# Performance work log

Hardware: AMD Instinct MI355X
Metric: run time of the kernel (lower is better)

Reference implementation:

```python
import jax, jax.numpy as jnp
import numpy as np

N, F, H, K = 8192, 128, 128, 16
E = N * 32


def _mlp(f, w1, b1, w2, b2, w3, b3):
    h = jax.nn.relu(f @ w1 + b1)
    h = jax.nn.relu(h @ w2 + b2)
    return h @ w3 + b3


def _edge_conv(x, w1, b1, w2, b2, w3, b3, k):
    # dynamic kNN in feature space (includes self like torch_cluster.knn with x==y)
    sn = jnp.sum(x * x, axis=1)
    d = sn[:, None] + sn[None, :] - 2.0 * (x @ x.T)  # [N,N] squared dists
    idx = jax.lax.top_k(-d, k)[1]                    # [N,k] nearest neighbors
    xj = x[idx]                                      # [N,k,H]
    xi = jnp.broadcast_to(x[:, None, :], xj.shape)
    f = jnp.concatenate([xi, xj - xi], axis=-1)      # [N,k,2H]
    return jnp.max(_mlp(f, w1, b1, w2, b2, w3, b3), axis=1)  # max aggregation


def _gcn(x, w, b, src, dst, norm, n):
    h = x @ w
    out = jax.ops.segment_sum(norm[:, None] * h[src], dst, num_segments=n)
    return out + b


def _forward(x, edge_index, edge_weight,
             wg1, bg1, wg2, bg2, wg3, bg3,
             e1w1, e1b1, e1w2, e1b2, e1w3, e1b3,
             e2w1, e2b1, e2w2, e2b2, e2w3, e2b3,
             e3w1, e3b1, e3w2, e3b2, e3w3, e3b3):
    n = x.shape[0]
    loop = jnp.arange(n)
    src = jnp.concatenate([edge_index[0], loop])  # source j
    dst = jnp.concatenate([edge_index[1], loop])  # target i
    ew = jnp.concatenate([edge_weight, jnp.ones((n,), x.dtype)])  # self-loop weight 1
    deg = jax.ops.segment_sum(ew, dst, num_segments=n)
    dis = jnp.where(deg > 0, jax.lax.rsqrt(jnp.maximum(deg, 1e-12)), 0.0)
    norm = dis[src] * ew * dis[dst]

    n1 = jnp.tanh(_gcn(x, wg1, bg1, src, dst, norm, n))   # dropout is identity at eval
    e1 = _edge_conv(n1, e1w1, e1b1, e1w2, e1b2, e1w3, e1b3, K)
    e1_n1 = jnp.linalg.norm(e1 + n1, axis=1, keepdims=True)  # [N,1]

    n2 = jnp.tanh(_gcn(n1, wg2, bg2, src, dst, norm, n))
    e2 = _edge_conv(n2, e2w1, e2b1, e2w2, e2b2, e2w3, e2b3, K)
    e2_n2 = e2 + n2

    n3 = jnp.tanh(_gcn(n2, wg3, bg3, src, dst, norm, n))
    e3 = _edge_conv(n3, e3w1, e3b1, e3w2, e3b2, e3w3, e3b3, K)
    e3_n3 = e3 + n3

    x2 = e1_n1 * e2_n2 * e3_n3
    return jax.nn.log_softmax(x2, axis=1)


def setup_inputs() -> dict:
    key = jax.random.key(0)
    ks = jax.random.split(key, 32)
    inp = {
        'x': jax.random.normal(ks[0], (N, F), dtype=jnp.float32),
        'edge_index': jax.random.randint(ks[1], (2, E), 0, N, dtype=jnp.int64) if jax.config.jax_enable_x64 else jax.random.randint(ks[1], (2, E), 0, N).astype(jnp.int32),
        'edge_weight': jax.random.uniform(ks[2], (E,), dtype=jnp.float32),
    }
    s = 0.05
    gcn_in = [F, H, H]
    for i in range(3):
        inp[f'wg{i+1}'] = jax.random.normal(ks[3 + i], (gcn_in[i], H), dtype=jnp.float32) * s
        inp[f'bg{i+1}'] = jnp.zeros((H,), jnp.float32)
    dims = [(2 * H, 64), (64, H), (H, H)]
    kk = 6
    for c in range(1, 4):
        for j, (di, do) in enumerate(dims):
            inp[f'e{c}w{j+1}'] = jax.random.normal(ks[kk], (di, do), dtype=jnp.float32) * s
            inp[f'e{c}b{j+1}'] = jnp.zeros((do,), jnp.float32)
            kk += 1
    return inp


def reference(x, edge_index, edge_weight,
              wg1, bg1, wg2, bg2, wg3, bg3,
              e1w1, e1b1, e1w2, e1b2, e1w3, e1b3,
              e2w1, e2b1, e2w2, e2b2, e2w3, e2b3,
              e3w1, e3b1, e3w2, e3b2, e3w3, e3b3):
    return _forward(x, edge_index, edge_weight,
                    wg1, bg1, wg2, bg2, wg3, bg3,
                    e1w1, e1b1, e1w2, e1b2, e1w3, e1b3,
                    e2w1, e2b1, e2w2, e2b2, e2w3, e2b3,
                    e3w1, e3b1, e3w2, e3b2, e3w3, e3b3)
```

## Files before the change

### kernel.cpp

```cpp
#include <hip/hip_runtime.h>
#include <math.h>

#define N_ 8192
#define H_ 128
#define E_ 262144
#define K_ 16
#define SLABJ 1024

typedef __attribute__((ext_vector_type(8))) short bshort8;
typedef __attribute__((ext_vector_type(16))) float f32x16;
typedef unsigned long long u64;

__global__ void k_deg_init(float* deg) {
  int i = blockIdx.x * 256 + threadIdx.x;
  deg[i] = 1.0f;
}

__global__ void k_deg_scatter(const int* __restrict__ ei, const float* __restrict__ ew,
                              float* deg) {
  int e = blockIdx.x * 256 + threadIdx.x;
  atomicAdd(&deg[ei[E_ + e]], ew[e]);
}

__global__ void k_dis(float* deg) {
  int i = blockIdx.x * 256 + threadIdx.x;
  deg[i] = rsqrtf(deg[i]);
}

__global__ void k_hist(const int* __restrict__ ei, int* hist) {
  int e = blockIdx.x * 256 + threadIdx.x;
  atomicAdd(&hist[ei[E_ + e]], 1);
}

__global__ void k_scan(int* hist, int* rowptr) {
  __shared__ int part[256];
  __shared__ int partx[257];
  int t = threadIdx.x;
  int base = t * 32;
  int loc[32];
  int s = 0;
#pragma unroll
  for (int i = 0; i < 32; ++i) { loc[i] = s; s += hist[base + i]; }
  part[t] = s;
  __syncthreads();
  if (t == 0) {
    int r = 0;
    for (int i = 0; i < 256; ++i) { partx[i] = r; r += part[i]; }
    partx[256] = r;
  }
  __syncthreads();
  int b = partx[t];
#pragma unroll
  for (int i = 0; i < 32; ++i) {
    rowptr[base + i] = b + loc[i];
    hist[base + i] = b + loc[i];
  }
  if (t == 0) rowptr[N_] = partx[256];
}

__global__ void k_edgebuild(const int* __restrict__ ei, const float* __restrict__ ew,
                            const float* __restrict__ dis, int* cursor,
                            int* __restrict__ srcS, float* __restrict__ normS) {
  int e = blockIdx.x * 256 + threadIdx.x;
  int s = ei[e], d = ei[E_ + e];
  int pos = atomicAdd(&cursor[d], 1);
  srcS[pos] = s;
  normS[pos] = dis[s] * ew[e] * dis[d];
}

__device__ __forceinline__ unsigned short f2bf_rne(float x) {
  unsigned u = __builtin_bit_cast(unsigned, x);
  unsigned r = ((u >> 16) & 1u) + 0x7fffu;
  return (unsigned short)((u + r) >> 16);
}
__device__ __forceinline__ float bf2f(unsigned short b) {
  unsigned u = ((unsigned)b) << 16;
  return __builtin_bit_cast(float, u);
}

struct WP { const float* p[12]; };

__global__ void k_wprepAll(WP wp, bshort8* __restrict__ wAll) {
  int id = blockIdx.x * 256 + threadIdx.x;
  int layer = id / 7168;
  int r = id - layer * 7168;
  bshort8* base = wAll + layer * 14336;
  const float* src;
  bshort8 *dH, *dL;
  int slot, kind;
  if (r < 2048)      { kind = 0; slot = r;        src = wp.p[layer*4+0]; dH = base;         dL = base + 2048; }
  else if (r < 4096) { kind = 1; slot = r - 2048; src = wp.p[layer*4+1]; dH = base + 4096;  dL = base + 6144; }
  else if (r < 5120) { kind = 2; slot = r - 4096; src = wp.p[layer*4+2]; dH = base + 8192;  dL = base + 9216; }
  else               { kind = 3; slot = r - 5120; src = wp.p[layer*4+3]; dH = base + 10240; dL = base + 12288; }
  int lane = slot & 63;
  int n, k0;
  if (kind == 2) {
    int ks = (slot >> 6) & 3, nt = slot >> 8;
    n = nt * 32 + (lane & 31);
    k0 = ks * 16 + (lane >> 5) * 8;
  } else {
    int ks = (slot >> 6) & 7, nt = slot >> 9;
    n = nt * 32 + (lane & 31);
    k0 = ks * 16 + (lane >> 5) * 8;
  }
  bshort8 h, l;
#pragma unroll
  for (int i = 0; i < 8; ++i) {
    int k = k0 + i;
    float v;
    if (kind == 1) v = (n < 64) ? (src[k * 64 + n] - src[(128 + k) * 64 + n])
                                : src[(128 + k) * 64 + (n - 64)];
    else v = src[k * 128 + n];
    unsigned short hb = f2bf_rne(v);
    h[i] = (short)hb;
    l[i] = (short)f2bf_rne(v - bf2f(hb));
  }
  dH[slot] = h;
  dL[slot] = l;
}

__global__ __launch_bounds__(256, 3) void k_gemmM(const float* __restrict__ A,
                                                  const bshort8* __restrict__ wfH,
                                                  const bshort8* __restrict__ wfL,
                                                  float* __restrict__ C) {
  __shared__ short aHs[32 * 132], aLs[32 * 132];
  int t = threadIdx.x;
  int r0 = blockIdx.x * 32;
  int w = t >> 6, lane = t & 63, q = lane & 31, half = lane >> 5;

  {
    int r = t >> 3;
    int kc = (t & 7) * 16;
    const float* p = A + (r0 + r) * 128 + kc;
#pragma unroll
    for (int e4 = 0; e4 < 4; ++e4) {
      float4 v = *(const float4*)(p + e4 * 4);
      float vals[4] = {v.x, v.y, v.z, v.w};
      unsigned short hs[4], ls[4];
#pragma unroll
      for (int i = 0; i < 4; ++i) {
        hs[i] = f2bf_rne(vals[i]);
        ls[i] = f2bf_rne(vals[i] - bf2f(hs[i]));
      }
      int off = r * 132 + kc + e4 * 4;
      *(u64*)&aHs[off] = ((u64)hs[0]) | ((u64)hs[1] << 16) | ((u64)hs[2] << 32) | ((u64)hs[3] << 48);
      *(u64*)&aLs[off] = ((u64)ls[0]) | ((u64)ls[1] << 16) | ((u64)ls[2] << 32) | ((u64)ls[3] << 48);
    }
  }
  bshort8 bH[8], bL[8];
#pragma unroll
  for (int ks = 0; ks < 8; ++ks) {
    bH[ks] = wfH[(w * 8 + ks) * 64 + lane];
    bL[ks] = wfL[(w * 8 + ks) * 64 + lane];
  }
  __syncthreads();

  f32x16 accP, accQ;
#pragma unroll
  for (int r = 0; r < 16; ++r) { accP[r] = 0.f; accQ[r] = 0.f; }
#pragma unroll
  for (int ks = 0; ks < 8; ++ks) {
    int off = q * 132 + ks * 16 + half * 8;
    union { bshort8 v; u64 u[2]; } aH, aL;
    aH.u[0] = *(const u64*)&aHs[off];
    aH.u[1] = *(const u64*)&aHs[off + 4];
    aL.u[0] = *(const u64*)&aLs[off];
    aL.u[1] = *(const u64*)&aLs[off + 4];
    accQ = __builtin_amdgcn_mfma_f32_32x32x16_bf16(aL.v, bH[ks], accQ, 0, 0, 0);
    accQ = __builtin_amdgcn_mfma_f32_32x32x16_bf16(aH.v, bL[ks], accQ, 0, 0, 0);
    accP = __builtin_amdgcn_mfma_f32_32x32x16_bf16(aH.v, bH[ks], accP, 0, 0, 0);
  }
#pragma unroll
  for (int reg = 0; reg < 16; ++reg) {
    int row = (reg & 3) + 8 * (reg >> 2) + 4 * half;
    C[(r0 + row) * 128 + w * 32 + q] = accP[reg] + accQ[reg];
  }
}

__global__ void k_gemmMF(const bshort8* __restrict__ fAH, const bshort8* __restrict__ fAL,
                         const bshort8* __restrict__ wfH, const bshort8* __restrict__ wfL,
                         float* __restrict__ C) {
  int t = threadIdx.x;
  int rt = blockIdx.x >> 1;
  int w = (blockIdx.x & 1) * 2 + (t >> 6);
  int lane = t & 63, q = lane & 31, half = lane >> 5;

  bshort8 bH[8], bL[8], aH[8], aL[8];
#pragma unroll
  for (int ks = 0; ks < 8; ++ks) {
    bH[ks] = wfH[(w * 8 + ks) * 64 + lane];
    bL[ks] = wfL[(w * 8 + ks) * 64 + lane];
    aH[ks] = fAH[(rt * 8 + ks) * 64 + lane];
    aL[ks] = fAL[(rt * 8 + ks) * 64 + lane];
  }
  f32x16 accP, accQ;
#pragma unroll
  for (int r = 0; r < 16; ++r) { accP[r] = 0.f; accQ[r] = 0.f; }
#pragma unroll
  for (int ks = 0; ks < 8; ++ks) {
    accQ = __builtin_amdgcn_mfma_f32_32x32x16_bf16(aL[ks], bH[ks], accQ, 0, 0, 0);
    accQ = __builtin_amdgcn_mfma_f32_32x32x16_bf16(aH[ks], bL[ks], accQ, 0, 0, 0);
    accP = __builtin_amdgcn_mfma_f32_32x32x16_bf16(aH[ks], bH[ks], accP, 0, 0, 0);
  }
#pragma unroll
  for (int reg = 0; reg < 16; ++reg) {
    int row = (reg & 3) + 8 * (reg >> 2) + 4 * half;
    C[(rt * 32 + row) * 128 + w * 32 + q] = accP[reg] + accQ[reg];
  }
}

__global__ __launch_bounds__(256) void k_gcn_agg(const float* __restrict__ h,
                                                 const float* __restrict__ dis,
                                                 const int* __restrict__ rowptr,
                                                 const int* __restrict__ srcS,
                                                 const float* __restrict__ normS,
                                                 const float* __restrict__ bg,
                                                 float* __restrict__ n_out,
                                                 float* __restrict__ sn) {
  __shared__ float part[4];
  int t = threadIdx.x;
  int i = blockIdx.x * 2 + (t >> 7);
  int c = t & 127;
  float di = dis[i];
  float a0 = di * di * h[i * 128 + c], a1 = 0.f, a2 = 0.f, a3 = 0.f;
  int e0 = rowptr[i], e1 = rowptr[i + 1];
  int e = e0;
  for (; e + 4 <= e1; e += 4) {
    int s0 = srcS[e], s1 = srcS[e + 1], s2 = srcS[e + 2], s3 = srcS[e + 3];
    float w0 = normS[e], w1 = normS[e + 1], w2 = normS[e + 2], w3 = normS[e + 3];
    a0 += w0 * h[s0 * 128 + c];
    a1 += w1 * h[s1 * 128 + c];
    a2 += w2 * h[s2 * 128 + c];
    a3 += w3 * h[s3 * 128 + c];
  }
  for (; e < e1; ++e) a0 += normS[e] * h[srcS[e] * 128 + c];
  float v = tanhf(a0 + a1 + a2 + a3 + bg[c]);
  n_out[i * 128 + c] = v;
  float vv = v * v;
#pragma unroll
  for (int off = 32; off; off >>= 1) vv += __shfl_down(vv, off, 64);
  if ((t & 63) == 0) part[t >> 6] = vv;
  __syncthreads();
  if ((t & 127) == 0) sn[i] = part[t >> 6] + part[(t >> 6) + 1];
}

__global__ void k_fragprep(const float* __restrict__ src, bshort8* __restrict__ hiA,
                           bshort8* __restrict__ loA) {
  int t = blockIdx.x * 256 + threadIdx.x;
  int j = t >> 4, slot = t & 15;
  const float* p = src + j * 128 + slot * 8;
  float4 f0 = *(const float4*)p;
  float4 f1 = *(const float4*)(p + 4);
  float f[8] = {f0.x, f0.y, f0.z, f0.w, f1.x, f1.y, f1.z, f1.w};
  bshort8 h, l;
#pragma unroll
  for (int i = 0; i < 8; ++i) {
    unsigned short hb = f2bf_rne(f[i]);
    h[i] = (short)hb;
    l[i] = (short)f2bf_rne(f[i] - bf2f(hb));
  }
  int ks = slot >> 1, half = slot & 1;
  int dst = ((j >> 5) * 8 + ks) * 64 + half * 32 + (j & 31);
  hiA[dst] = h;
  loA[dst] = l;
}

__device__ __forceinline__ u64 packkey(float d, int j) {
  unsigned m = __builtin_bit_cast(unsigned, d);
  m = (m & 0x80000000u) ? ~m : (m | 0x80000000u);
  return (((u64)m) << 32) | (unsigned)j;
}

__device__ __forceinline__ float unpackd(u64 key) {
  unsigned m = (unsigned)(key >> 32);
  unsigned u = (m & 0x80000000u) ? (m & 0x7fffffffu) : ~m;
  return __builtin_bit_cast(float, u);
}

__device__ __forceinline__ void ins8(u64* tk, u64 x) {
  bool c[8];
#pragma unroll
  for (int s = 0; s < 8; ++s) c[s] = x < tk[s];
#pragma unroll
  for (int s = 7; s >= 1; --s) tk[s] = c[s - 1] ? tk[s - 1] : (c[s] ? x : tk[s]);
  tk[0] = c[0] ? x : tk[0];
}

__device__ __forceinline__ void ins16(u64* tk, u64 x) {
  bool c[16];
#pragma unroll
  for (int s = 0; s < 16; ++s) c[s] = x < tk[s];
#pragma unroll
  for (int s = 15; s >= 1; --s) tk[s] = c[s - 1] ? tk[s - 1] : (c[s] ? x : tk[s]);
  tk[0] = c[0] ? x : tk[0];
}

__global__ __launch_bounds__(256, 3) void k_knnA(const bshort8* __restrict__ fragHi,
                                                 const bshort8* __restrict__ fragLo,
                                                 const float* __restrict__ sn,
                                                 u64* __restrict__ candR) {
  __shared__ float snS[SLABJ];
  int t = threadIdx.x;
  int qtile = blockIdx.x, chunk = blockIdx.y;
  int wave = t >> 6, lane = t & 63;
  int q = lane & 31, half = lane >> 5;

#pragma unroll
  for (int p = 0; p < 4; ++p) snS[t + 256 * p] = sn[chunk * SLABJ + t + 256 * p];

  bshort8 bHi[8], bLo[8];
#pragma unroll
  for (int ks = 0; ks < 8; ++ks) {
    int o = (qtile * 8 + ks) * 64 + lane;
    bHi[ks] = fragHi[o];
    bLo[ks] = fragLo[o];
  }
  __syncthreads();

  u64 tk[8];
#pragma unroll
  for (int s = 0; s < 8; ++s) tk[s] = ~0ULL;

  for (int ti = 0; ti < 8; ++ti) {
    int jt = chunk * 32 + wave * 8 + ti;
    f32x16 accP, accQ;
#pragma unroll
    for (int r = 0; r < 16; ++r) { accP[r] = 0.f; accQ[r] = 0.f; }
    {
      bshort8 aH[4], aL[4];
#pragma unroll
      for (int k4 = 0; k4 < 4; ++k4) {
        int o = (jt * 8 + k4) * 64 + lane;
        aH[k4] = fragHi[o];
        aL[k4] = fragLo[o];
      }
#pragma unroll
      for (int k4 = 0; k4 < 4; ++k4) {
        accQ = __builtin_amdgcn_mfma_f32_32x32x16_bf16(aL[k4], bHi[k4], accQ, 0, 0, 0);
        accQ = __builtin_amdgcn_mfma_f32_32x32x16_bf16(aH[k4], bLo[k4], accQ, 0, 0, 0);
        accP = __builtin_amdgcn_mfma_f32_32x32x16_bf16(aH[k4], bHi[k4], accP, 0, 0, 0);
      }
    }
    {
      bshort8 aH[4], aL[4];
#pragma unroll
      for (int k4 = 0; k4 < 4; ++k4) {
        int o = (jt * 8 + 4 + k4) * 64 + lane;
        aH[k4] = fragHi[o];
        aL[k4] = fragLo[o];
      }
#pragma unroll
      for (int k4 = 0; k4 < 4; ++k4) {
        accQ = __builtin_amdgcn_mfma_f32_32x32x16_bf16(aL[k4], bHi[4 + k4], accQ, 0, 0, 0);
        accQ = __builtin_amdgcn_mfma_f32_32x32x16_bf16(aH[k4], bLo[4 + k4], accQ, 0, 0, 0);
        accP = __builtin_amdgcn_mfma_f32_32x32x16_bf16(aH[k4], bHi[4 + k4], accP, 0, 0, 0);
      }
    }

    int jbase = (wave * 8 + ti) * 32;
#pragma unroll
    for (int rp = 0; rp < 8; ++rp) {
      int r0 = rp * 2;
      int row0 = (r0 & 3) + 8 * (r0 >> 2) + 4 * half;
      float d0 = snS[jbase + row0] - 2.0f * (accP[r0] + accQ[r0]);
      float d1 = snS[jbase + row0 + 1] - 2.0f * (accP[r0 + 1] + accQ[r0 + 1]);
      u64 k0 = packkey(d0, chunk * SLABJ + jbase + row0);
      u64 k1 = packkey(d1, chunk * SLABJ + jbase + row0 + 1);
      u64 km = k0 < k1 ? k0 : k1;
      if (km < tk[7]) {
        if (k0 < tk[7]) ins8(tk, k0);
        if (k1 < tk[7]) ins8(tk, k1);
      }
    }
  }

  int g = wave * 2 + half;
#pragma unroll
  for (int s = 0; s < 8; ++s)
    candR[(size_t)(chunk * 64 + g * 8 + s) * N_ + qtile * 32 + q] = tk[s];
}

__global__ __launch_bounds__(256) void k_tauseedX(const u64* __restrict__ candR,
                                                  u64* __restrict__ accept,
                                                  int* __restrict__ cursor,
                                                  u64* __restrict__ tauKey,
                                                  float* __restrict__ tauD) {
  __shared__ u64 mb[64 * 65];
  int t = threadIdx.x;
  int ql = t >> 2, j = t & 3;
  int q = blockIdx.x * 64 + ql;

  int rb[4];
#pragma unroll
  for (int k = 0; k < 4; ++k) {
    int L = 4 * j + k;
    rb[k] = (L >> 3) * 64 + (L & 7) * 8;
  }
  int h0 = 0, h1 = 0, h2 = 0, h3 = 0;
  for (int step = 0; step < 16; ++step) {
    u64 best = (h0 < 8) ? candR[(size_t)(rb[0] + h0) * N_ + q] : ~0ULL;
    int bg = 0;
    u64 b;
    b = (h1 < 8) ? candR[(size_t)(rb[1] + h1) * N_ + q] : ~0ULL; if (b < best) { best = b; bg = 1; }
    b = (h2 < 8) ? candR[(size_t)(rb[2] + h2) * N_ + q] : ~0ULL; if (b < best) { best = b; bg = 2; }
    b = (h3 < 8) ? candR[(size_t)(rb[3] + h3) * N_ + q] : ~0ULL; if (b < best) { best = b; bg = 3; }
    mb[ql * 65 + j * 16 + step] = best;
    h0 += (bg == 0); h1 += (bg == 1); h2 += (bg == 2); h3 += (bg == 3);
  }
  __syncthreads();
  if (t < 64) {
    int qq = blockIdx.x * 64 + t;
    int base = t * 65;
    int g0 = 0, g1 = 0, g2 = 0, g3 = 0;
    u64 best = 0;
    for (int step = 0; step < 16; ++step) {
      best = mb[base + g0];
      int bg = 0;
      u64 b;
      b = mb[base + 16 + g1]; if (b < best) { best = b; bg = 1; }
      b = mb[base + 32 + g2]; if (b < best) { best = b; bg = 2; }
      b = mb[base + 48 + g3]; if (b < best) { best = b; bg = 3; }
      accept[(size_t)step * N_ + qq] = best;
      g0 += (bg == 0); g1 += (bg == 1); g2 += (bg == 2); g3 += (bg == 3);
    }
    tauKey[qq] = best;
    tauD[qq] = unpackd(best);
    cursor[qq] = 16;
  }
}

__global__ __launch_bounds__(256, 3) void k_knnB(const bshort8* __restrict__ fragHi,
                                                 const bshort8* __restrict__ fragLo,
                                                 const float* __restrict__ sn,
                                                 const float* __restrict__ tauD,
                                                 int* __restrict__ cursor,
                                                 u64* __restrict__ accept,
                                                 u64* __restrict__ accExt) {
  __shared__ float snS[SLABJ];
  int t = threadIdx.x;
  int qtile = blockIdx.x, slab = blockIdx.y + 2;
  int wave = t >> 6, lane = t & 63;
  int q = lane & 31, half = lane >> 5;
  int qg = qtile * 32 + q;

#pragma unroll
  for (int p = 0; p < 4; ++p) snS[t + 256 * p] = sn[slab * SLABJ + t + 256 * p];

  bshort8 bHi[8], bLo[8];
#pragma unroll
  for (int ks = 0; ks < 8; ++ks) {
    int o = (qtile * 8 + ks) * 64 + lane;
    bHi[ks] = fragHi[o];
    bLo[ks] = fragLo[o];
  }
  float tD = tauD[qg];
  __syncthreads();

  u64 buf[6];
  int cnt = 0;

  for (int ti = 0; ti < 8; ++ti) {
    int jt = slab * 32 + wave * 8 + ti;
    f32x16 accP, accQ;
#pragma unroll
    for (int r = 0; r < 16; ++r) { accP[r] = 0.f; accQ[r] = 0.f; }
    {
      bshort8 aH[4], aL[4];
#pragma unroll
      for (int k4 = 0; k4 < 4; ++k4) {
        int o = (jt * 8 + k4) * 64 + lane;
        aH[k4] = fragHi[o];
        aL[k4] = fragLo[o];
      }
#pragma unroll
      for (int k4 = 0; k4 < 4; ++k4) {
        accQ = __builtin_amdgcn_mfma_f32_32x32x16_bf16(aL[k4], bHi[k4], accQ, 0, 0, 0);
        accQ = __builtin_amdgcn_mfma_f32_32x32x16_bf16(aH[k4], bLo[k4], accQ, 0, 0, 0);
        accP = __builtin_amdgcn_mfma_f32_32x32x16_bf16(aH[k4], bHi[k4], accP, 0, 0, 0);
      }
    }
    {
      bshort8 aH[4], aL[4];
#pragma unroll
      for (int k4 = 0; k4 < 4; ++k4) {
        int o = (jt * 8 + 4 + k4) * 64 + lane;
        aH[k4] = fragHi[o];
        aL[k4] = fragLo[o];
      }
#pragma unroll
      for (int k4 = 0; k4 < 4; ++k4) {
        accQ = __builtin_amdgcn_mfma_f32_32x32x16_bf16(aL[k4], bHi[4 + k4], accQ, 0, 0, 0);
        accQ = __builtin_amdgcn_mfma_f32_32x32x16_bf16(aH[k4], bLo[4 + k4], accQ, 0, 0, 0);
        accP = __builtin_amdgcn_mfma_f32_32x32x16_bf16(aH[k4], bHi[4 + k4], accP, 0, 0, 0);
      }
    }

    int jbase = (wave * 8 + ti) * 32;
#pragma unroll
    for (int rp = 0; rp < 8; ++rp) {
      int r0 = rp * 2;
      int row0 = (r0 & 3) + 8 * (r0 >> 2) + 4 * half;
      float d0 = snS[jbase + row0] - 2.0f * (accP[r0] + accQ[r0]);
      float d1 = snS[jbase + row0 + 1] - 2.0f * (accP[r0 + 1] + accQ[r0 + 1]);
      if (d0 <= tD) {
        u64 k0 = packkey(d0, slab * SLABJ + jbase + row0);
        if (cnt < 6) {
#pragma unroll
          for (int s = 0; s < 6; ++s)
            if (s == cnt) buf[s] = k0;
          ++cnt;
        } else {
          int pos = atomicAdd(&cursor[qg], 1);
          if (pos < 128) accept[(size_t)pos * N_ + qg] = k0;
          else if (pos < 192) accExt[(size_t)(pos - 128) * N_ + qg] = k0;
        }
      }
      if (d1 <= tD) {
        u64 k1 = packkey(d1, slab * SLABJ + jbase + row0 + 1);
        if (cnt < 6) {
#pragma unroll
          for (int s = 0; s < 6; ++s)
            if (s == cnt) buf[s] = k1;
          ++cnt;
        } else {
          int pos = atomicAdd(&cursor[qg], 1);
          if (pos < 128) accept[(size_t)pos * N_ + qg] = k1;
          else if (pos < 192) accExt[(size_t)(pos - 128) * N_ + qg] = k1;
        }
      }
    }
  }

  if (cnt > 0) {
    int pos = atomicAdd(&cursor[qg], cnt);
#pragma unroll
    for (int s = 0; s < 6; ++s) {
      if (s < cnt) {
        int slot = pos + s;
        if (slot < 128) accept[(size_t)slot * N_ + qg] = buf[s];
        else if (slot < 192) accExt[(size_t)(slot - 128) * N_ + qg] = buf[s];
      }
    }
  }
}

__global__ __launch_bounds__(256) void k_select(const u64* __restrict__ accept,
                                                const u64* __restrict__ accExt,
                                                const int* __restrict__ cursor,
                                                int* __restrict__ idxo) {
  __shared__ u64 mb[64 * 65];
  int t = threadIdx.x;
  int ql = t >> 2;
  int j = t & 3;
  int q = blockIdx.x * 64 + ql;
  int c = cursor[q];
  if (c > 192) c = 192;
  u64 tk[16];
#pragma unroll
  for (int s = 0; s < 16; ++s) tk[s] = ~0ULL;
  for (int i = j; i < c; i += 4) {
    u64 x = (i < 128) ? accept[(size_t)i * N_ + q] : accExt[(size_t)(i - 128) * N_ + q];
    if (x < tk[15]) ins16(tk, x);
  }
#pragma unroll
  for (int s = 0; s < 16; ++s) mb[ql * 65 + j * 16 + s] = tk[s];
  __syncthreads();
  if (t < 64) {
    int qq = blockIdx.x * 64 + t;
    int base = t * 65;
    int h0 = 0, h1 = 0, h2 = 0, h3 = 0;
    for (int step = 0; step < 16; ++step) {
      u64 best = mb[base + h0];
      int bg = 0;
      u64 b;
      b = mb[base + 16 + h1]; if (b < best) { best = b; bg = 1; }
      b = mb[base + 32 + h2]; if (b < best) { best = b; bg = 2; }
      b = mb[base + 48 + h3]; if (b < best) { best = b; bg = 3; }
      idxo[qq * 16 + step] = (int)(unsigned)(best & 0xffffffffULL);
      h0 += (bg == 0); h1 += (bg == 1); h2 += (bg == 2); h3 += (bg == 3);
    }
  }
}

__global__ __launch_bounds__(256, 3) void k_mlpM(
    const float* __restrict__ ab, const int* __restrict__ idx,
    const bshort8* __restrict__ w2fH, const bshort8* __restrict__ w2fL,
    const bshort8* __restrict__ w3fH, const bshort8* __restrict__ w3fL,
    const float* __restrict__ b1g, const float* __restrict__ b2g,
    const float* __restrict__ b3g, const float* __restrict__ nadd,
    float* __restrict__ eout) {
  __shared__ short h1H[64 * 68], h1L[64 * 68];
  __shared__ short h2H[64 * 132], h2L[64 * 132];
  int t = threadIdx.x;
  int n0 = blockIdx.x * 4;
  int w = t >> 6, lane = t & 63, q = lane & 31, half = lane >> 5;

  {
    int r = t >> 2;
    int kc = (t & 3) * 16;
    int node = n0 + (r >> 4);
    int jn = idx[node * 16 + (r & 15)];
    const float* pa = ab + node * 128 + kc;
    const float* pb = ab + jn * 128 + 64 + kc;
    const float* p1 = b1g + kc;
#pragma unroll
    for (int e4 = 0; e4 < 4; ++e4) {
      float4 va = *(const float4*)(pa + e4 * 4);
      float4 vb = *(const float4*)(pb + e4 * 4);
      float4 v1 = *(const float4*)(p1 + e4 * 4);
      float vals[4] = {va.x + vb.x + v1.x, va.y + vb.y + v1.y,
                       va.z + vb.z + v1.z, va.w + vb.w + v1.w};
      unsigned short hs[4], ls[4];
#pragma unroll
      for (int i = 0; i < 4; ++i) {
        float v = fmaxf(vals[i], 0.f);
        hs[i] = f2bf_rne(v);
        ls[i] = f2bf_rne(v - bf2f(hs[i]));
      }
      int off = r * 68 + kc + e4 * 4;
      *(u64*)&h1H[off] = ((u64)hs[0]) | ((u64)hs[1] << 16) | ((u64)hs[2] << 32) | ((u64)hs[3] << 48);
      *(u64*)&h1L[off] = ((u64)ls[0]) | ((u64)ls[1] << 16) | ((u64)ls[2] << 32) | ((u64)ls[3] << 48);
    }
  }

  bshort8 c2H[4], c2L[4];
#pragma unroll
  for (int ks = 0; ks < 4; ++ks) {
    c2H[ks] = w2fH[(w * 4 + ks) * 64 + lane];
    c2L[ks] = w2fL[(w * 4 + ks) * 64 + lane];
  }
  bshort8 c3H[8], c3L[8];
#pragma unroll
  for (int ks = 0; ks < 8; ++ks) {
    c3H[ks] = w3fH[(w * 8 + ks) * 64 + lane];
    c3L[ks] = w3fL[(w * 8 + ks) * 64 + lane];
  }
  float bias2 = b2g[w * 32 + q];
  float bias3 = b3g[w * 32 + q];
  __syncthreads();

#pragma unroll
  for (int rt = 0; rt < 2; ++rt) {
    f32x16 acc;
#pragma unroll
    for (int r = 0; r < 16; ++r) acc[r] = 0.f;
#pragma unroll
    for (int ks = 0; ks < 4; ++ks) {
      int off = (rt * 32 + q) * 68 + ks * 16 + half * 8;
      union { bshort8 v; u64 u[2]; } aH, aL;
      aH.u[0] = *(const u64*)&h1H[off];
      aH.u[1] = *(const u64*)&h1H[off + 4];
      aL.u[0] = *(const u64*)&h1L[off];
      aL.u[1] = *(const u64*)&h1L[off + 4];
      acc = __builtin_amdgcn_mfma_f32_32x32x16_bf16(aL.v, c2H[ks], acc, 0, 0, 0);
      acc = __builtin_amdgcn_mfma_f32_32x32x16_bf16(aH.v, c2L[ks], acc, 0, 0, 0);
      acc = __builtin_amdgcn_mfma_f32_32x32x16_bf16(aH.v, c2H[ks], acc, 0, 0, 0);
    }
#pragma unroll
    for (int reg = 0; reg < 16; ++reg) {
      int row = rt * 32 + (reg & 3) + 8 * (reg >> 2) + 4 * half;
      float v = fmaxf(acc[reg] + bias2, 0.f);
      unsigned short hb = f2bf_rne(v);
      h2H[row * 132 + w * 32 + q] = (short)hb;
      h2L[row * 132 + w * 32 + q] = (short)f2bf_rne(v - bf2f(hb));
    }
  }
  __syncthreads();

#pragma unroll
  for (int rt = 0; rt < 2; ++rt) {
    f32x16 acc;
#pragma unroll
    for (int r = 0; r < 16; ++r) acc[r] = 0.f;
#pragma unroll
    for (int ks = 0; ks < 8; ++ks) {
      int off = (rt * 32 + q) * 132 + ks * 16 + half * 8;
      union { bshort8 v; u64 u[2]; } aH, aL;
      aH.u[0] = *(const u64*)&h2H[off];
      aH.u[1] = *(const u64*)&h2H[off + 4];
      aL.u[0] = *(const u64*)&h2L[off];
      aL.u[1] = *(const u64*)&h2L[off + 4];
      acc = __builtin_amdgcn_mfma_f32_32x32x16_bf16(aL.v, c3H[ks], acc, 0, 0, 0);
      acc = __builtin_amdgcn_mfma_f32_32x32x16_bf16(aH.v, c3L[ks], acc, 0, 0, 0);
      acc = __builtin_amdgcn_mfma_f32_32x32x16_bf16(aH.v, c3H[ks], acc, 0, 0, 0);
    }
    float mA = -INFINITY, mB = -INFINITY;
#pragma unroll
    for (int reg = 0; reg < 8; ++reg) mA = fmaxf(mA, acc[reg]);
#pragma unroll
    for (int reg = 8; reg < 16; ++reg) mB = fmaxf(mB, acc[reg]);
    mA = fmaxf(mA, __shfl_xor(mA, 32, 64));
    mB = fmaxf(mB, __shfl_xor(mB, 32, 64));
    int col = w * 32 + q;
    int nodeA = n0 + rt * 2, nodeB = n0 + rt * 2 + 1;
    if (half == 0) {
      float v = mA + bias3;
      if (nadd) v += nadd[nodeA * 128 + col];
      eout[nodeA * 128 + col] = v;
    } else {
      float v = mB + bias3;
      if (nadd) v += nadd[nodeB * 128 + col];
      eout[nodeB * 128 + col] = v;
    }
  }
}

__global__ void k_e1n1(const float* __restrict__ e1, const float* __restrict__ n1,
                       float* s1) {
  int t = threadIdx.x;
  int node = blockIdx.x * 4 + (t >> 6);
  int lane = t & 63;
  float v0 = e1[node * 128 + lane] + n1[node * 128 + lane];
  float v1 = e1[node * 128 + 64 + lane] + n1[node * 128 + 64 + lane];
  float ss = v0 * v0 + v1 * v1;
#pragma unroll
  for (int off = 32; off; off >>= 1) ss += __shfl_down(ss, off, 64);
  if (lane == 0) s1[node] = sqrtf(ss);
}

__global__ void k_final(const float* __restrict__ s1, const float* __restrict__ e2n2,
                        const float* __restrict__ e3n3, float* __restrict__ out) {
  int t = threadIdx.x;
  int node = blockIdx.x * 4 + (t >> 6);
  int lane = t & 63;
  float s = s1[node];
  float z0 = s * e2n2[node * 128 + lane] * e3n3[node * 128 + lane];
  float z1 = s * e2n2[node * 128 + 64 + lane] * e3n3[node * 128 + 64 + lane];
  float m = fmaxf(z0, z1);
#pragma unroll
  for (int off = 32; off; off >>= 1) m = fmaxf(m, __shfl_xor(m, off, 64));
  float ex = expf(z0 - m) + expf(z1 - m);
#pragma unroll
  for (int off = 32; off; off >>= 1) ex += __shfl_xor(ex, off, 64);
  float lse = m + logf(ex);
  out[node * 128 + lane] = z0 - lse;
  out[node * 128 + 64 + lane] = z1 - lse;
}

extern "C" void kernel_launch(void* const* d_in, const int* in_sizes, int n_in,
                              void* d_out, int out_size, void* d_ws, size_t ws_size,
                              hipStream_t stream) {
  (void)in_sizes; (void)n_in; (void)out_size;
  const float* x  = (const float*)d_in[0];
  const int* ei   = (const int*)d_in[1];
  const float* ew = (const float*)d_in[2];
  const float* wg[3] = {(const float*)d_in[3], (const float*)d_in[5], (const float*)d_in[7]};
  const float* bg[3] = {(const float*)d_in[4], (const float*)d_in[6], (const float*)d_in[8]};
  const float* ew1[3] = {(const float*)d_in[9],  (const float*)d_in[15], (const float*)d_in[21]};
  const float* eb1[3] = {(const float*)d_in[10], (const float*)d_in[16], (const float*)d_in[22]};
  const float* ew2[3] = {(const float*)d_in[11], (const float*)d_in[17], (const float*)d_in[23]};
  const float* eb2[3] = {(const float*)d_in[12], (const float*)d_in[18], (const float*)d_in[24]};
  const float* ew3[3] = {(const float*)d_in[13], (const float*)d_in[19], (const float*)d_in[25]};
  const float* eb3[3] = {(const float*)d_in[14], (const float*)d_in[20], (const float*)d_in[26]};

  size_t small = (size_t)(23 * N_ + (N_ + 256) + N_ + 2 * E_);
  size_t need = (small + 172032 + (size_t)7 * N_ * H_) * sizeof(float);
  if (ws_size < need) return;

  float* ws  = (float*)d_ws;
  float* dis = ws;
  float* sn  = ws + N_;
  float* S1  = ws + 2 * N_;
  int* idx   = (int*)(ws + 3 * N_);
  u64* tauKey = (u64*)(ws + 19 * N_);
  int* cursor = (int*)(ws + 21 * N_);
  float* tauD = ws + 22 * N_;
  int* rowptr = (int*)(ws + 23 * N_);
  int* hist   = rowptr + N_ + 256;
  int* srcS   = hist + N_;
  float* normS = (float*)(srcS + E_);
  bshort8* wAll = (bshort8*)(normS + E_);
  float* h   = (float*)(normS + E_ + 172032);
  float* n1  = h + N_ * H_;
  float* n2  = n1 + N_ * H_;
  float* n3  = n2 + N_ * H_;
  float* E2  = n3 + N_ * H_;
  float* E1  = E2 + N_ * H_;
  float* ab  = E1 + N_ * H_;

  bshort8* fragHi = (bshort8*)h;
  bshort8* fragLo = (bshort8*)(h + N_ * H_ / 2);
  u64* candR  = (u64*)E1;
  u64* accept = (u64*)E1;

  float* nl[3] = {n1, n2, n3};
  float* spare[3] = {n2, n1, n2};
  float* nadd[3] = {nullptr, n2, n3};

  k_deg_init<<<N_ / 256, 256, 0, stream>>>(dis);
  k_deg_scatter<<<E_ / 256, 256, 0, stream>>>(ei, ew, dis);
  k_dis<<<N_ / 256, 256, 0, stream>>>(dis);
  hipMemsetAsync(hist, 0, N_ * sizeof(int), stream);
  k_hist<<<E_ / 256, 256, 0, stream>>>(ei, hist);
  k_scan<<<1, 256, 0, stream>>>(hist, rowptr);
  k_edgebuild<<<E_ / 256, 256, 0, stream>>>(ei, ew, dis, hist, srcS, normS);

  WP wp;
  for (int l = 0; l < 3; ++l) {
    wp.p[l * 4 + 0] = wg[l];
    wp.p[l * 4 + 1] = ew1[l];
    wp.p[l * 4 + 2] = ew2[l];
    wp.p[l * 4 + 3] = ew3[l];
  }
  k_wprepAll<<<84, 256, 0, stream>>>(wp, wAll);

  for (int l = 0; l < 3; ++l) {
    bshort8* wl = wAll + l * 14336;
    bshort8* wgfH = wl;            bshort8* wgfL = wl + 2048;
    bshort8* w1fH = wl + 4096;     bshort8* w1fL = wl + 6144;
    bshort8* w2fH = wl + 8192;     bshort8* w2fL = wl + 9216;
    bshort8* w3fH = wl + 10240;    bshort8* w3fL = wl + 12288;

    const float* inp = (l == 0) ? x : nl[l - 1];
    k_gemmM<<<256, 256, 0, stream>>>(inp, wgfH, wgfL, h);
    k_gcn_agg<<<N_ / 2, 256, 0, stream>>>(h, dis, rowptr, srcS, normS, bg[l], nl[l], sn);
    k_fragprep<<<N_ * 16 / 256, 256, 0, stream>>>(nl[l], fragHi, fragLo);
    k_knnA<<<dim3(N_ / 32, 2), 256, 0, stream>>>(fragHi, fragLo, sn, candR);
    k_tauseedX<<<N_ / 64, 256, 0, stream>>>(candR, accept, cursor, tauKey, tauD);
    k_knnB<<<dim3(N_ / 32, 6), 256, 0, stream>>>(fragHi, fragLo, sn, tauD, cursor,
                                                 accept, (u64*)spare[l]);
    k_select<<<N_ / 64, 256, 0, stream>>>(accept, (u64*)spare[l], cursor, idx);
    k_gemmMF<<<512, 128, 0, stream>>>(fragHi, fragLo, w1fH, w1fL, ab);
    float* etgt = (l == 1) ? E2 : E1;
    k_mlpM<<<N_ / 4, 256, 0, stream>>>(ab, idx, w2fH, w2fL, w3fH, w3fL,
                                       eb1[l], eb2[l], eb3[l], nadd[l], etgt);
    if (l == 0) k_e1n1<<<N_ / 4, 256, 0, stream>>>(E1, n1, S1);
  }
  k_final<<<N_ / 4, 256, 0, stream>>>(S1, E2, E1, (float*)d_out);
}
```

Measured before the change: 817.6 us.

## Seed kNN threshold from sampled subset and rescan all slabs in pass B

Pass A now covers only the first 2048 candidates, split into four 512-wide chunks with top-4 lists per group, and only estimates the threshold tau. Pass B then rescans all eight slabs, including the ones pass A saw, and collects every candidate under tau, with the accept list starting empty. The aim is a cheaper seeding pass with smaller insertion networks and more parallel blocks. The cost is a recomputation of the first 2048 distances in pass B and a looser tau, since it comes from fewer candidates, which could make more candidates pass the filter and grow the overflow work.

```diff
diff --git a/kernel.cpp b/kernel.cpp
--- a/kernel.cpp
+++ b/kernel.cpp
@@ -6,6 +6,7 @@
 #define E_ 262144
 #define K_ 16
 #define SLABJ 1024
+#define CHUNKJ 512
 
 typedef __attribute__((ext_vector_type(8))) short bshort8;
 typedef __attribute__((ext_vector_type(16))) float f32x16;
@@ -277,12 +278,12 @@
   return __builtin_bit_cast(float, u);
 }
 
-__device__ __forceinline__ void ins8(u64* tk, u64 x) {
-  bool c[8];
-#pragma unroll
-  for (int s = 0; s < 8; ++s) c[s] = x < tk[s];
-#pragma unroll
-  for (int s = 7; s >= 1; --s) tk[s] = c[s - 1] ? tk[s - 1] : (c[s] ? x : tk[s]);
+__device__ __forceinline__ void ins4(u64* tk, u64 x) {
+  bool c[4];
+#pragma unroll
+  for (int s = 0; s < 4; ++s) c[s] = x < tk[s];
+#pragma unroll
+  for (int s = 3; s >= 1; --s) tk[s] = c[s - 1] ? tk[s - 1] : (c[s] ? x : tk[s]);
   tk[0] = c[0] ? x : tk[0];
 }
 
@@ -299,14 +300,14 @@
                                                  const bshort8* __restrict__ fragLo,
                                                  const float* __restrict__ sn,
                                                  u64* __restrict__ candR) {
-  __shared__ float snS[SLABJ];
+  __shared__ float snS[CHUNKJ];
   int t = threadIdx.x;
   int qtile = blockIdx.x, chunk = blockIdx.y;
   int wave = t >> 6, lane = t & 63;
   int q = lane & 31, half = lane >> 5;
 
-#pragma unroll
-  for (int p = 0; p < 4; ++p) snS[t + 256 * p] = sn[chunk * SLABJ + t + 256 * p];
+  snS[t] = sn[chunk * CHUNKJ + t];
+  snS[t + 256] = sn[chunk * CHUNKJ + t + 256];
 
   bshort8 bHi[8], bLo[8];
 #pragma unroll
@@ -317,12 +318,12 @@
   }
   __syncthreads();
 
-  u64 tk[8];
-#pragma unroll
-  for (int s = 0; s < 8; ++s) tk[s] = ~0ULL;
-
-  for (int ti = 0; ti < 8; ++ti) {
-    int jt = chunk * 32 + wave * 8 + ti;
+  u64 tk[4];
+#pragma unroll
+  for (int s = 0; s < 4; ++s) tk[s] = ~0ULL;
+
+  for (int ti = 0; ti < 4; ++ti) {
+    int jt = chunk * 16 + wave * 4 + ti;
     f32x16 accP, accQ;
 #pragma unroll
     for (int r = 0; r < 16; ++r) { accP[r] = 0.f; accQ[r] = 0.f; }
@@ -357,55 +358,58 @@
       }
     }
 
-    int jbase = (wave * 8 + ti) * 32;
+    int jbase = (wave * 4 + ti) * 32;
 #pragma unroll
     for (int rp = 0; rp < 8; ++rp) {
       int r0 = rp * 2;
       int row0 = (r0 & 3) + 8 * (r0 >> 2) + 4 * half;
       float d0 = snS[jbase + row0] - 2.0f * (accP[r0] + accQ[r0]);
       float d1 = snS[jbase + row0 + 1] - 2.0f * (accP[r0 + 1] + accQ[r0 + 1]);
-      u64 k0 = packkey(d0, chunk * SLABJ + jbase + row0);
-      u64 k1 = packkey(d1, chunk * SLABJ + jbase + row0 + 1);
+      u64 k0 = packkey(d0, chunk * CHUNKJ + jbase + row0);
+      u64 k1 = packkey(d1, chunk * CHUNKJ + jbase + row0 + 1);
       u64 km = k0 < k1 ? k0 : k1;
-      if (km < tk[7]) {
-        if (k0 < tk[7]) ins8(tk, k0);
-        if (k1 < tk[7]) ins8(tk, k1);
+      if (km < tk[3]) {
+        if (k0 < tk[3]) ins4(tk, k0);
+        if (k1 < tk[3]) ins4(tk, k1);
       }
     }
   }
 
   int g = wave * 2 + half;
 #pragma unroll
-  for (int s = 0; s < 8; ++s)
-    candR[(size_t)(chunk * 64 + g * 8 + s) * N_ + qtile * 32 + q] = tk[s];
+  for (int s = 0; s < 4; ++s)
+    candR[(size_t)(chunk * 32 + g * 4 + s) * N_ + qtile * 32 + q] = tk[s];
 }
 
 __global__ __launch_bounds__(256) void k_tauseedX(const u64* __restrict__ candR,
-                                                  u64* __restrict__ accept,
                                                   int* __restrict__ cursor,
-                                                  u64* __restrict__ tauKey,
                                                   float* __restrict__ tauD) {
   __shared__ u64 mb[64 * 65];
   int t = threadIdx.x;
   int ql = t >> 2, j = t & 3;
   int q = blockIdx.x * 64 + ql;
 
-  int rb[4];
-#pragma unroll
-  for (int k = 0; k < 4; ++k) {
-    int L = 4 * j + k;
-    rb[k] = (L >> 3) * 64 + (L & 7) * 8;
-  }
-  int h0 = 0, h1 = 0, h2 = 0, h3 = 0;
+  int rb[8];
+#pragma unroll
+  for (int k = 0; k < 8; ++k) {
+    int L = 8 * j + k;
+    rb[k] = (L >> 3) * 32 + (L & 7) * 4;
+  }
+  int h0 = 0, h1 = 0, h2 = 0, h3 = 0, h4 = 0, h5 = 0, h6 = 0, h7 = 0;
   for (int step = 0; step < 16; ++step) {
-    u64 best = (h0 < 8) ? candR[(size_t)(rb[0] + h0) * N_ + q] : ~0ULL;
+    u64 best = (h0 < 4) ? candR[(size_t)(rb[0] + h0) * N_ + q] : ~0ULL;
     int bg = 0;
     u64 b;
-    b = (h1 < 8) ? candR[(size_t)(rb[1] + h1) * N_ + q] : ~0ULL; if (b < best) { best = b; bg = 1; }
-    b = (h2 < 8) ? candR[(size_t)(rb[2] + h2) * N_ + q] : ~0ULL; if (b < best) { best = b; bg = 2; }
-    b = (h3 < 8) ? candR[(size_t)(rb[3] + h3) * N_ + q] : ~0ULL; if (b < best) { best = b; bg = 3; }
+    b = (h1 < 4) ? candR[(size_t)(rb[1] + h1) * N_ + q] : ~0ULL; if (b < best) { best = b; bg = 1; }
+    b = (h2 < 4) ? candR[(size_t)(rb[2] + h2) * N_ + q] : ~0ULL; if (b < best) { best = b; bg = 2; }
+    b = (h3 < 4) ? candR[(size_t)(rb[3] + h3) * N_ + q] : ~0ULL; if (b < best) { best = b; bg = 3; }
+    b = (h4 < 4) ? candR[(size_t)(rb[4] + h4) * N_ + q] : ~0ULL; if (b < best) { best = b; bg = 4; }
+    b = (h5 < 4) ? candR[(size_t)(rb[5] + h5) * N_ + q] : ~0ULL; if (b < best) { best = b; bg = 5; }
+    b = (h6 < 4) ? candR[(size_t)(rb[6] + h6) * N_ + q] : ~0ULL; if (b < best) { best = b; bg = 6; }
+    b = (h7 < 4) ? candR[(size_t)(rb[7] + h7) * N_ + q] : ~0ULL; if (b < best) { best = b; bg = 7; }
     mb[ql * 65 + j * 16 + step] = best;
     h0 += (bg == 0); h1 += (bg == 1); h2 += (bg == 2); h3 += (bg == 3);
+    h4 += (bg == 4); h5 += (bg == 5); h6 += (bg == 6); h7 += (bg == 7);
   }
   __syncthreads();
   if (t < 64) {
@@ -420,12 +424,10 @@
       b = mb[base + 16 + g1]; if (b < best) { best = b; bg = 1; }
       b = mb[base + 32 + g2]; if (b < best) { best = b; bg = 2; }
       b = mb[base + 48 + g3]; if (b < best) { best = b; bg = 3; }
-      accept[(size_t)step * N_ + qq] = best;
       g0 += (bg == 0); g1 += (bg == 1); g2 += (bg == 2); g3 += (bg == 3);
     }
-    tauKey[qq] = best;
     tauD[qq] = unpackd(best);
-    cursor[qq] = 16;
+    cursor[qq] = 0;
   }
 }
 
@@ -438,7 +440,7 @@
                                                  u64* __restrict__ accExt) {
   __shared__ float snS[SLABJ];
   int t = threadIdx.x;
-  int qtile = blockIdx.x, slab = blockIdx.y + 2;
+  int qtile = blockIdx.x, slab = blockIdx.y;
   int wave = t >> 6, lane = t & 63;
   int q = lane & 31, half = lane >> 5;
   int qg = qtile * 32 + q;
@@ -762,7 +764,6 @@
   float* sn  = ws + N_;
   float* S1  = ws + 2 * N_;
   int* idx   = (int*)(ws + 3 * N_);
-  u64* tauKey = (u64*)(ws + 19 * N_);
   int* cursor = (int*)(ws + 21 * N_);
   float* tauD = ws + 22 * N_;
   int* rowptr = (int*)(ws + 23 * N_);
@@ -815,9 +816,9 @@
     k_gemmM<<<256, 256, 0, stream>>>(inp, wgfH, wgfL, h);
     k_gcn_agg<<<N_ / 2, 256, 0, stream>>>(h, dis, rowptr, srcS, normS, bg[l], nl[l], sn);
     k_fragprep<<<N_ * 16 / 256, 256, 0, stream>>>(nl[l], fragHi, fragLo);
-    k_knnA<<<dim3(N_ / 32, 2), 256, 0, stream>>>(fragHi, fragLo, sn, candR);
-    k_tauseedX<<<N_ / 64, 256, 0, stream>>>(candR, accept, cursor, tauKey, tauD);
-    k_knnB<<<dim3(N_ / 32, 6), 256, 0, stream>>>(fragHi, fragLo, sn, tauD, cursor,
+    k_knnA<<<dim3(N_ / 32, 4), 256, 0, stream>>>(fragHi, fragLo, sn, candR);
+    k_tauseedX<<<N_ / 64, 256, 0, stream>>>(candR, cursor, tauD);
+    k_knnB<<<dim3(N_ / 32, 8), 256, 0, stream>>>(fragHi, fragLo, sn, tauD, cursor,
                                                  accept, (u64*)spare[l]);
     k_select<<<N_ / 64, 256, 0, stream>>>(accept, (u64*)spare[l], cursor, idx);
     k_gemmMF<<<512, 128, 0, stream>>>(fragHi, fragLo, w1fH, w1fL, ab);
```

Result: no change. 823.5 us (+0.7%).
